# Performance work log

Hardware: AMD Instinct MI355X
Metric: run time of the kernel (lower is better)

## Reference

```python
import jax, jax.numpy as jnp
import numpy as np

K = 10
NUM_BLKS = 6
LN_EPS = 1e-6
NODE_D = 64


def layer_norm(x, g, b):
    m = jnp.mean(x, axis=-1, keepdims=True)
    v = jnp.var(x, axis=-1, keepdims=True)
    return (x - m) * jax.lax.rsqrt(v + LN_EPS) * g + b


def setup_inputs() -> dict:
    key = jax.random.key(0)
    B, N_c, N_t, D_S, D_F = 4, 4096, 1024, 3, 4
    D_IN = 4 + D_S + D_F  # obs-embed(4) + s + f
    ks = jax.random.split(key, 32)
    sc = 0.02
    inp = {
        "s_ctx": jax.random.normal(ks[0], (B, N_c, D_S), jnp.float32),
        "f_ctx": jax.random.normal(ks[1], (B, N_c, D_F), jnp.float32),
        "s_test": jax.random.normal(ks[2], (B, N_t, D_S), jnp.float32),
        "valid_lens_ctx": jax.random.randint(ks[3], (B,), N_c // 2, N_c + 1).astype(jnp.int32),
        # embed_obs: nn.Embed(2, 4)
        "emb_obs": jax.random.normal(ks[4], (2, 4), jnp.float32) * sc,
        # embed_all: MLP([256,128,64], gelu)
        "ea_W0": jax.random.normal(ks[5], (D_IN, 256), jnp.float32) * sc, "ea_b0": jnp.zeros((256,), jnp.float32),
        "ea_W1": jax.random.normal(ks[6], (256, 128), jnp.float32) * sc, "ea_b1": jnp.zeros((128,), jnp.float32),
        "ea_W2": jax.random.normal(ks[7], (128, NODE_D), jnp.float32) * sc, "ea_b2": jnp.zeros((NODE_D,), jnp.float32),
        # top-level LayerNorm
        "ln_g": jnp.ones((NODE_D,), jnp.float32), "ln_b": jnp.zeros((NODE_D,), jnp.float32),
        # GraphKRBlock params, stacked over NUM_BLKS blocks
        "blk_Wm0": jax.random.normal(ks[8], (NUM_BLKS, NODE_D + 1, 128), jnp.float32) * sc,
        "blk_bm0": jnp.zeros((NUM_BLKS, 128), jnp.float32),
        "blk_Wm1": jax.random.normal(ks[9], (NUM_BLKS, 128, NODE_D), jnp.float32) * sc,
        "blk_bm1": jnp.zeros((NUM_BLKS, NODE_D), jnp.float32),
        "blk_Wu0": jax.random.normal(ks[10], (NUM_BLKS, 2 * NODE_D, 128), jnp.float32) * sc,
        "blk_bu0": jnp.zeros((NUM_BLKS, 128), jnp.float32),
        "blk_Wu1": jax.random.normal(ks[11], (NUM_BLKS, 128, NODE_D), jnp.float32) * sc,
        "blk_bu1": jnp.zeros((NUM_BLKS, NODE_D), jnp.float32),
        "blk_lng": jnp.ones((NUM_BLKS, NODE_D), jnp.float32),
        "blk_lnb": jnp.zeros((NUM_BLKS, NODE_D), jnp.float32),
        # head: MLP([256,64,2], gelu)
        "hd_W0": jax.random.normal(ks[12], (NODE_D, 256), jnp.float32) * sc, "hd_b0": jnp.zeros((256,), jnp.float32),
        "hd_W1": jax.random.normal(ks[13], (256, 64), jnp.float32) * sc, "hd_b1": jnp.zeros((64,), jnp.float32),
        "hd_W2": jax.random.normal(ks[14], (64, 2), jnp.float32) * sc, "hd_b2": jnp.zeros((2,), jnp.float32),
    }
    return inp


def reference(s_ctx, f_ctx, s_test, valid_lens_ctx,
              emb_obs, ea_W0, ea_b0, ea_W1, ea_b1, ea_W2, ea_b2, ln_g, ln_b,
              blk_Wm0, blk_bm0, blk_Wm1, blk_bm1, blk_Wu0, blk_bu0, blk_Wu1, blk_bu1,
              blk_lng, blk_lnb, hd_W0, hd_b0, hd_W1, hd_b1, hd_W2, hd_b2):
    B, N_c, _ = s_ctx.shape
    N_t = s_test.shape[1]

    # --- per-sample O(n^2) KNN graph build (custom_k_nearest_senders, l2 dist) ---
    mask = jnp.arange(N_c)[None, :] < valid_lens_ctx[:, None]          # [B,N_c]
    s_send = jnp.where(mask[..., None], s_ctx, 1e6)                    # invalid -> far away
    rx = jnp.concatenate([s_ctx, s_test], axis=1)                      # [B,N,d_s] receivers
    d = jnp.sqrt(jnp.sum((rx[:, :, None, :] - s_send[:, None, :, :]) ** 2, axis=-1))  # [B,N,N_c]
    negd, senders = jax.lax.top_k(-d, K)                               # k-nearest: [B,N,K]
    dists = -negd                                                       # ascending distances

    # --- embeddings: stack(embed_obs, s, f) -> embed_all MLP -> LayerNorm ---
    def embed(x):
        h = jax.nn.gelu(x @ ea_W0 + ea_b0)
        h = jax.nn.gelu(h @ ea_W1 + ea_b1)
        h = h @ ea_W2 + ea_b2
        return layer_norm(h, ln_g, ln_b)

    ctx_in = jnp.concatenate(
        [jnp.broadcast_to(emb_obs[1], (B, N_c, emb_obs.shape[1])), s_ctx, f_ctx], axis=-1)
    test_in = jnp.concatenate(
        [jnp.broadcast_to(emb_obs[0], (B, N_t, emb_obs.shape[1])), s_test,
         jnp.zeros((B, N_t, f_ctx.shape[-1]), f_ctx.dtype)], axis=-1)
    nodes = jnp.concatenate([embed(ctx_in), embed(test_in)], axis=1)   # [B,N,64]

    # --- num_blks GraphKRBlock message-passing blocks ---
    bidx = jnp.arange(B)[:, None, None]
    w = jax.nn.softmax(-dists, axis=-1)                                # kernel weights per receiver
    for i in range(NUM_BLKS):
        sf = nodes[bidx, senders]                                      # gather senders [B,N,K,64]
        m_in = jnp.concatenate([sf, dists[..., None]], axis=-1)        # [B,N,K,65]
        m = jax.nn.gelu(m_in @ blk_Wm0[i] + blk_bm0[i]) @ blk_Wm1[i] + blk_bm1[i]
        agg = jnp.einsum('bnk,bnkd->bnd', w, m)                        # scatter-to-receivers
        u_in = jnp.concatenate([nodes, agg], axis=-1)                  # [B,N,128]
        upd = jax.nn.gelu(u_in @ blk_Wu0[i] + blk_bu0[i]) @ blk_Wu1[i] + blk_bu1[i]
        nodes = layer_norm(nodes + upd, blk_lng[i], blk_lnb[i])

    # --- head on test nodes ---
    x_t = nodes[:, N_c:, :]                                            # [B,N_t,64]
    h = jax.nn.gelu(x_t @ hd_W0 + hd_b0)
    h = jax.nn.gelu(h @ hd_W1 + hd_b1)
    f_dist = h @ hd_W2 + hd_b2                                         # [B,N_t,2]
    f_mu, f_log_var = jnp.split(f_dist, 2, axis=-1)
    f_std = jnp.exp(f_log_var / 2)                                     # min_std = 0.0
    return f_mu, f_std
```

## Files before the change

### kernel.cpp

```cpp
#include <hip/hip_runtime.h>
#include <math.h>

#define BB 4
#define NC 4096
#define NT 1024
#define NN (NC + NT)
#define NODES (BB * NN)
#define DD 64
#define KNN 10
#define NBLK 6
#define BIGF 3.0e38f

typedef __attribute__((ext_vector_type(8))) short short8;
typedef __attribute__((ext_vector_type(4))) float f32x4;
typedef __attribute__((ext_vector_type(4))) int int4v;

__device__ __forceinline__ unsigned short f2bf(float f) {
    unsigned int u = __float_as_uint(f);
    unsigned int r = (u + 0x7fffu + ((u >> 16) & 1u)) >> 16;
    return (unsigned short)r;
}
__device__ __forceinline__ float bf2f(unsigned short h) {
    return __uint_as_float(((unsigned int)h) << 16);
}

__device__ __forceinline__ float gelu_f(float x) {
    const float c0 = 0.7978845608028654f;
    float x3 = x * x * x;
    float z2 = 2.0f * c0 * (x + 0.044715f * x3);
    float e = __expf(z2);
    float r = __builtin_amdgcn_rcpf(1.0f + e);
    return x - x * r;
}

__device__ __forceinline__ float wave_sum(float v) {
#pragma unroll
    for (int off = 32; off > 0; off >>= 1) v += __shfl_xor(v, off, 64);
    return v;
}

__device__ __forceinline__ f32x4 mfma_bf16(short8 a, short8 b, f32x4 c) {
    asm("v_mfma_f32_16x16x32_bf16 %0, %1, %2, %0" : "+v"(c) : "v"(a), "v"(b));
    return c;
}


__global__ __launch_bounds__(256) void k_convw(
    const float* __restrict__ Wm0, const float* __restrict__ Wm1,
    const float* __restrict__ Wu0, const float* __restrict__ Wu1,
    const float* __restrict__ bm0,
    const float* __restrict__ eW0, const float* __restrict__ eW1,
    const float* __restrict__ eW2,
    const float* __restrict__ hW0, const float* __restrict__ hW1,
    const float* __restrict__ sctx,
    unsigned short* __restrict__ wtm0, unsigned short* __restrict__ wtm1p,
    unsigned short* __restrict__ wtu0, unsigned short* __restrict__ wtu1,
    float* __restrict__ wdp, float* __restrict__ bm0p,
    unsigned short* __restrict__ wte0, unsigned short* __restrict__ wte1,
    unsigned short* __restrict__ wte2,
    unsigned short* __restrict__ wth0, unsigned short* __restrict__ wth1,
    float4* __restrict__ s4)
{
    int t = blockIdx.x * 256 + threadIdx.x;
    if (t < 49152) {
        int i = t / 8192, r = t % 8192, n = r / 64, k = r % 64;
        wtm0[t] = f2bf(Wm0[(i * 65 + k) * 128 + n]);
    } else if (t < 98304) {
        int u = t - 49152;
        int i = u / 8192, r = u % 8192, n = r / 128, cp = r % 128;
        int col = ((cp & 7) << 4) | (cp >> 3);
        wtm1p[u] = f2bf(Wm1[(i * 128 + col) * 64 + n]);
    } else if (t < 196608) {
        int u = t - 98304;
        int i = u / 16384, r = u % 16384, n = r / 128, k = r % 128;
        wtu0[u] = f2bf(Wu0[(i * 128 + k) * 128 + n]);
    } else if (t < 245760) {
        int u = t - 196608;
        int i = u / 8192, r = u % 8192, n = r / 128, k = r % 128;
        wtu1[u] = f2bf(Wu1[(i * 128 + k) * 64 + n]);
    } else if (t < 246528) {
        int u = t - 245760;
        int i = u / 128, cp = u % 128;
        int col = ((cp & 7) << 4) | (cp >> 3);
        wdp[u] = Wm0[(i * 65 + 64) * 128 + col];
    } else if (t < 247296) {
        int u = t - 246528;
        int i = u / 128, cp = u % 128;
        int col = ((cp & 7) << 4) | (cp >> 3);
        bm0p[u] = bm0[i * 128 + col];
    } else if (t < 255488) {
        int u = t - 247296;
        int n = u / 32, k = u % 32;
        wte0[u] = (k < 11) ? f2bf(eW0[k * 256 + n]) : 0;
    } else if (t < 288256) {
        int u = t - 255488;
        int n = u / 256, k = u % 256;
        wte1[u] = f2bf(eW1[k * 128 + n]);
    } else if (t < 296448) {
        int u = t - 288256;
        int n = u / 128, k = u % 128;
        wte2[u] = f2bf(eW2[k * 64 + n]);
    } else if (t < 312832) {
        int u = t - 296448;
        int n = u / 64, k = u % 64;
        wth0[u] = f2bf(hW0[k * 256 + n]);
    } else if (t < 329216) {
        int u = t - 312832;
        int n = u / 256, k = u % 256;
        wth1[u] = f2bf(hW1[k * 64 + n]);
    } else if (t < 329216 + BB * NC) {
        int u = t - 329216;
        float x = sctx[u * 3], y = sctx[u * 3 + 1], z = sctx[u * 3 + 2];
        s4[u] = make_float4(x, y, z, 0.0f);
    }
}

__global__ __launch_bounds__(256) void k_embed2(
    const float* __restrict__ s_ctx, const float* __restrict__ f_ctx,
    const float* __restrict__ s_test, const float* __restrict__ emb_obs,
    const unsigned short* __restrict__ WT0, const float* __restrict__ b0,
    const unsigned short* __restrict__ WT1, const float* __restrict__ b1,
    const unsigned short* __restrict__ WT2, const float* __restrict__ b2,
    const float* __restrict__ g, const float* __restrict__ bta,
    const unsigned short* __restrict__ Wm0n,
    unsigned short* __restrict__ nodes,
    unsigned short* __restrict__ Pout)
{
    __shared__ unsigned short H0[4][16 * 256];
    __shared__ unsigned short H1[4][16 * 128];
    __shared__ unsigned short XO[4][16 * 64];
    int t = threadIdx.x;
    int wave = t >> 6, lane = t & 63, lr = lane & 15, lk = lane >> 4;
    int rb = wave * 16;
    int n0 = blockIdx.x * 64;
    int bq = n0 / NN, nloc0 = n0 % NN;
    bool is_ctx = nloc0 < NC;
    int nr = nloc0 + rb + lr;
    float xv[8];
#pragma unroll
    for (int j = 0; j < 8; ++j) xv[j] = 0.0f;
    if (lk == 0) {
        const float* eb = emb_obs + (is_ctx ? 4 : 0);
        xv[0] = eb[0]; xv[1] = eb[1]; xv[2] = eb[2]; xv[3] = eb[3];
        if (is_ctx) {
            const float* sp = s_ctx + ((size_t)(bq * NC + nr)) * 3;
            const float* fp = f_ctx + ((size_t)(bq * NC + nr)) * 4;
            xv[4] = sp[0]; xv[5] = sp[1]; xv[6] = sp[2]; xv[7] = fp[0];
        } else {
            const float* sp = s_test + ((size_t)(bq * NT + nr - NC)) * 3;
            xv[4] = sp[0]; xv[5] = sp[1]; xv[6] = sp[2];
        }
    } else if (lk == 1 && is_ctx) {
        const float* fp = f_ctx + ((size_t)(bq * NC + nr)) * 4;
        xv[0] = fp[1]; xv[1] = fp[2]; xv[2] = fp[3];
    }
    short8 a;
#pragma unroll
    for (int j = 0; j < 8; ++j) a[j] = (short)f2bf(xv[j]);

    f32x4 acc0[16];
#pragma unroll
    for (int nt = 0; nt < 16; ++nt) {
        short8 bb = *(const short8*)(WT0 + (nt * 16 + lr) * 32 + lk * 8);
        f32x4 z = (f32x4){0.f, 0.f, 0.f, 0.f};
        acc0[nt] = mfma_bf16(a, bb, z);
    }
    unsigned short* h0 = &H0[wave][0];
#pragma unroll
    for (int nt = 0; nt < 16; ++nt) {
        int col = nt * 16 + lr;
        float bias = b0[col];
        int u = col >> 3;
#pragma unroll
        for (int j = 0; j < 4; ++j) {
            int row = lk * 4 + j;
            float v = gelu_f(acc0[nt][j] + bias);
            int us = (u & 16) | ((u ^ row) & 15);
            h0[row * 256 + us * 8 + (col & 7)] = f2bf(v);
        }
    }
    f32x4 acc1[8];
#pragma unroll
    for (int nt = 0; nt < 8; ++nt) acc1[nt] = (f32x4){0.f, 0.f, 0.f, 0.f};
#pragma unroll
    for (int ks = 0; ks < 8; ++ks) {
        int u = ks * 4 + lk;
        int us = (u & 16) | ((u ^ lr) & 15);
        short8 aa = *(const short8*)(&h0[lr * 256 + us * 8]);
#pragma unroll
        for (int nt = 0; nt < 8; ++nt) {
            short8 bb = *(const short8*)(WT1 + (nt * 16 + lr) * 256 + ks * 32 + lk * 8);
            acc1[nt] = mfma_bf16(aa, bb, acc1[nt]);
        }
    }
    unsigned short* h1 = &H1[wave][0];
#pragma unroll
    for (int nt = 0; nt < 8; ++nt) {
        int col = nt * 16 + lr;
        float bias = b1[col];
        int u = col >> 3;
#pragma unroll
        for (int j = 0; j < 4; ++j) {
            int row = lk * 4 + j;
            float v = gelu_f(acc1[nt][j] + bias);
            int us = (u ^ row) & 15;
            h1[row * 128 + us * 8 + (col & 7)] = f2bf(v);
        }
    }
    f32x4 acc2[4];
#pragma unroll
    for (int nt = 0; nt < 4; ++nt) acc2[nt] = (f32x4){0.f, 0.f, 0.f, 0.f};
#pragma unroll
    for (int ks = 0; ks < 4; ++ks) {
        int u = ks * 4 + lk;
        int us = (u ^ lr) & 15;
        short8 aa = *(const short8*)(&h1[lr * 128 + us * 8]);
#pragma unroll
        for (int nt = 0; nt < 4; ++nt) {
            short8 bb = *(const short8*)(WT2 + (nt * 16 + lr) * 128 + ks * 32 + lk * 8);
            acc2[nt] = mfma_bf16(aa, bb, acc2[nt]);
        }
    }
    float vals[4][4];
#pragma unroll
    for (int j = 0; j < 4; ++j)
#pragma unroll
        for (int nt = 0; nt < 4; ++nt)
            vals[j][nt] = acc2[nt][j] + b2[nt * 16 + lr];
    unsigned short* xo = &XO[wave][0];
#pragma unroll
    for (int j = 0; j < 4; ++j) {
        float s = vals[j][0] + vals[j][1] + vals[j][2] + vals[j][3];
#pragma unroll
        for (int m = 1; m < 16; m <<= 1) s += __shfl_xor(s, m, 64);
        float mean = s * (1.0f / 64.0f);
        float vs = 0.0f;
#pragma unroll
        for (int nt = 0; nt < 4; ++nt) { float d = vals[j][nt] - mean; vs += d * d; }
#pragma unroll
        for (int m = 1; m < 16; m <<= 1) vs += __shfl_xor(vs, m, 64);
        float inv = rsqrtf(vs * (1.0f / 64.0f) + 1e-6f);
        int row = lk * 4 + j;
        int node = n0 + rb + row;
#pragma unroll
        for (int nt = 0; nt < 4; ++nt) {
            int col = nt * 16 + lr;
            float o = (vals[j][nt] - mean) * inv * g[col] + bta[col];
            unsigned short ob = f2bf(o);
            nodes[(size_t)node * 64 + col] = ob;
            xo[row * 64 + ((col >> 3) ^ (row & 7)) * 8 + (col & 7)] = ob;
        }
    }
    f32x4 accP[8];
#pragma unroll
    for (int nt = 0; nt < 8; ++nt) accP[nt] = (f32x4){0.f, 0.f, 0.f, 0.f};
#pragma unroll
    for (int ks = 0; ks < 2; ++ks) {
        short8 aa = *(const short8*)(&xo[lr * 64 + ((ks * 4 + lk) ^ (lr & 7)) * 8]);
#pragma unroll
        for (int nt = 0; nt < 8; ++nt) {
            short8 bb = *(const short8*)(Wm0n + (nt * 16 + lr) * 64 + ks * 32 + lk * 8);
            accP[nt] = mfma_bf16(aa, bb, accP[nt]);
        }
    }
#pragma unroll
    for (int j = 0; j < 4; ++j) {
        int node = n0 + rb + lk * 4 + j;
        short8 ps;
#pragma unroll
        for (int nt = 0; nt < 8; ++nt) ps[nt] = (short)f2bf(accP[nt][j]);
        *(short8*)(Pout + (size_t)node * 128 + lr * 8) = ps;
    }
}

__global__ __launch_bounds__(256) void k_topk(
    const float4* __restrict__ s4, const float* __restrict__ s_ctx,
    const float* __restrict__ s_test, const int* __restrict__ valid_lens,
    float* __restrict__ dists, int* __restrict__ senders, float* __restrict__ wout)
{
    __shared__ float cd[4 * 64 * 11];
    __shared__ float seld[4][4][12];
    __shared__ int   seli[4][4][12];
    __shared__ int   eqis[4][4][12];
    int wave = threadIdx.x >> 6;
    int lane = threadIdx.x & 63;
    int r0 = blockIdx.x * 16 + wave * 4;
    int b = r0 / NN;
    int vl = valid_lens[b];
    const float4* sc = s4 + (size_t)b * NC;
    float px[4], py[4], pz[4];
#pragma unroll
    for (int q = 0; q < 4; ++q) {
        int n = (r0 + q) % NN;
        const float* p = (n < NC) ? &s_ctx[(size_t)(b * NC + n) * 3]
                                  : &s_test[(size_t)(b * NT + (n - NC)) * 3];
        px[q] = p[0]; py[q] = p[1]; pz[q] = p[2];
    }
    float bq[4][KNN];
#pragma unroll
    for (int q = 0; q < 4; ++q)
#pragma unroll
        for (int k = 0; k < KNN; ++k) bq[q][k] = BIGF;
#pragma unroll 8
    for (int i = 0; i < 64; ++i) {
        int j = lane + (i << 6);
        float4 s = sc[j];
        bool ok = j < vl;
#pragma unroll
        for (int q = 0; q < 4; ++q) {
            float dx = px[q] - s.x, dy = py[q] - s.y, dz = pz[q] - s.z;
            float d2 = fmaf(dx, dx, fmaf(dy, dy, dz * dz));
            d2 = ok ? d2 : BIGF;
#pragma unroll
            for (int k = KNN - 1; k >= 1; --k)
                bq[q][k] = __builtin_amdgcn_fmed3f(bq[q][k - 1], bq[q][k], d2);
            bq[q][0] = fminf(bq[q][0], d2);
        }
    }
    int base = (wave * 64 + lane) * 11;
    float T[4], dmin[4];
    int m[4];
#pragma unroll
    for (int q = 0; q < 4; ++q) {
#pragma unroll
        for (int k = 0; k < KNN; ++k) cd[base + k] = bq[q][k];
        __builtin_amdgcn_wave_barrier();
        int head = 0;
        float myd = 0.0f;
#pragma unroll
        for (int rr = 0; rr < KNN; ++rr) {
            float v = cd[base + head];
            float mv = v;
#pragma unroll
            for (int off = 32; off > 0; off >>= 1) mv = fminf(mv, __shfl_xor(mv, off, 64));
            unsigned long long ball = __ballot(v == mv);
            int win = __ffsll(ball) - 1;
            if (lane == win) head++;
            if (lane == rr) myd = mv;
        }
        T[q] = __shfl(myd, 9, 64);
        dmin[q] = sqrtf(__shfl(myd, 0, 64));
        m[q] = __popcll(__ballot(lane < KNN && myd < T[q]));
    }
    unsigned long long below = (lane == 63) ? 0x7FFFFFFFFFFFFFFFull
                                            : ((1ull << lane) - 1);
    int cless[4] = {0, 0, 0, 0}, ceq[4] = {0, 0, 0, 0};
#pragma unroll 4
    for (int i = 0; i < 64; ++i) {
        int j = lane + (i << 6);
        float4 s = sc[j];
        bool ok = j < vl;
#pragma unroll
        for (int q = 0; q < 4; ++q) {
            float dx = px[q] - s.x, dy = py[q] - s.y, dz = pz[q] - s.z;
            float v = fmaf(dx, dx, fmaf(dy, dy, dz * dz));
            v = ok ? v : BIGF;
            unsigned long long ml = __ballot(v < T[q]);
            unsigned long long me = __ballot(v == T[q]);
            if (v < T[q]) {
                int slot = cless[q] + __popcll(ml & below);
                if (slot < 12) { seld[wave][q][slot] = v; seli[wave][q][slot] = j; }
            }
            if (v == T[q]) {
                int qq = ceq[q] + __popcll(me & below);
                if (qq < 12) eqis[wave][q][qq] = j;
            }
            cless[q] += __popcll(ml);
            ceq[q] += __popcll(me);
        }
    }
    __builtin_amdgcn_wave_barrier();
#pragma unroll
    for (int q = 0; q < 4; ++q) {
        float e = 0.0f, d = 0.0f;
        int isel = 0;
        if (lane < KNN) {
            float vsel;
            if (lane < m[q]) { vsel = seld[wave][q][lane]; isel = seli[wave][q][lane]; }
            else             { vsel = T[q];                isel = eqis[wave][q][lane - m[q]]; }
            d = sqrtf(vsel);
            e = __expf(-(d - dmin[q]));
        }
        float ssum = wave_sum(e);
        if (lane < KNN) {
            size_t o = (size_t)(r0 + q) * KNN + lane;
            dists[o] = d;
            senders[o] = isel;
            wout[o] = e / ssum;
        }
    }
}

__global__ __launch_bounds__(256) void k_blk(
    const unsigned short* __restrict__ nodes_in,
    const unsigned short* __restrict__ P,
    const float* __restrict__ dists, const int* __restrict__ senders,
    const float* __restrict__ w,
    const float* __restrict__ wdp, const float* __restrict__ bm0p,
    const unsigned short* __restrict__ Wm1p,
    const float* __restrict__ bm1,
    const unsigned short* __restrict__ WTu0,
    const float* __restrict__ bu0,
    const unsigned short* __restrict__ WTu1,
    const float* __restrict__ bu1,
    const float* __restrict__ lng, const float* __restrict__ lnb,
    const unsigned short* __restrict__ Wm0n,
    const int doP,
    unsigned short* __restrict__ nodes_out,
    unsigned short* __restrict__ Pout)
{
    __shared__ unsigned short X[16 * 64];
    __shared__ unsigned short G[16 * 128];
    __shared__ unsigned short AG[16 * 64];
    __shared__ unsigned short H[16 * 128];
    __shared__ unsigned short XO[16 * 64];
    __shared__ int   sidE[160];
    __shared__ float dE[160], wE[160];
    int l = threadIdx.x;
    int wave = l >> 6, lane = l & 63;
    int n0 = blockIdx.x * 16;
    int b = n0 / NN;
    size_t bbase = (size_t)b * NN;
    int e0 = n0 * KNN;
    if (l < 160) {
        sidE[l] = senders[e0 + l];
        dE[l]   = dists[e0 + l];
        wE[l]   = w[e0 + l];
    }
    if (l < 128) {
        int row = l >> 3, u = l & 7;
        int4v v = *(const int4v*)(nodes_in + ((size_t)(n0 + row)) * 64 + u * 8);
        *(int4v*)(&X[row * 64 + (u ^ (row & 7)) * 8]) = v;
    }
    __syncthreads();
    float wd0 = wdp[2 * lane], wd1 = wdp[2 * lane + 1];
    float bb0 = bm0p[2 * lane], bb1 = bm0p[2 * lane + 1];
    const unsigned int* Pb = (const unsigned int*)P;
    unsigned int* G32 = (unsigned int*)G;
#pragma unroll
    for (int nn = 0; nn < 4; ++nn) {
        int n = wave * 4 + nn;
        float a0 = 0.0f, a1 = 0.0f;
#pragma unroll
        for (int k = 0; k < KNN; ++k) {
            int e = n * KNN + k;
            int sid = sidE[e];
            float dd = dE[e], ww = wE[e];
            unsigned int pr = Pb[(bbase + sid) * 64 + lane];
// ... 95 lines not shown
        for (int mm = 1; mm < 16; mm <<= 1) vs += __shfl_xor(vs, mm, 64);
        float inv = rsqrtf(vs * (1.0f / 64.0f) + 1e-6f);
#pragma unroll
        for (int nt = 0; nt < 4; ++nt) {
            int col = nt * 16 + lr;
            float o = (vals[j][nt] - mean) * inv * lng[col] + lnb[col];
            unsigned short ob = f2bf(o);
            nodes_out[((size_t)(n0 + row)) * 64 + col] = ob;
            XO[row * 64 + ((col >> 3) ^ (row & 7)) * 8 + (col & 7)] = ob;
        }
    }
    if (doP) {
        f32x4 accP[8];
#pragma unroll
        for (int nt = 0; nt < 8; ++nt) accP[nt] = (f32x4){0.f, 0.f, 0.f, 0.f};
#pragma unroll
        for (int ks = 0; ks < 2; ++ks) {
            short8 aa = *(const short8*)(&XO[lr * 64 + ((ks * 4 + lk) ^ (lr & 7)) * 8]);
#pragma unroll
            for (int nt = 0; nt < 8; ++nt) {
                short8 bb = *(const short8*)(Wm0n + (nt * 16 + lr) * 64 + ks * 32 + lk * 8);
                accP[nt] = mfma_bf16(aa, bb, accP[nt]);
            }
        }
#pragma unroll
        for (int j = 0; j < 4; ++j) {
            int node = n0 + lk * 4 + j;
            short8 ps;
#pragma unroll
            for (int nt = 0; nt < 8; ++nt) ps[nt] = (short)f2bf(accP[nt][j]);
            *(short8*)(Pout + (size_t)node * 128 + lr * 8) = ps;
        }
    }
}

__global__ __launch_bounds__(256) void k_head2(
    const unsigned short* __restrict__ nodes,
    const unsigned short* __restrict__ WT0, const float* __restrict__ b0,
    const unsigned short* __restrict__ WT1, const float* __restrict__ b1,
    const float* __restrict__ W2, const float* __restrict__ b2,
    float* __restrict__ out)
{
    __shared__ unsigned short H0[4][16 * 256];
    __shared__ unsigned short H1[4][16 * 72];
    int t = threadIdx.x;
    int wave = t >> 6, lane = t & 63, lr = lane & 15, lk = lane >> 4;
    int rb = wave * 16;
    int n0 = blockIdx.x * 64;
    int bq = n0 / NT, nloc0 = n0 % NT;
    size_t grow = (size_t)(bq * NN + NC + nloc0 + rb);
    short8 a0 = *(const short8*)(nodes + (grow + lr) * 64 + lk * 8);
    short8 a1 = *(const short8*)(nodes + (grow + lr) * 64 + 32 + lk * 8);
    f32x4 acc0[16];
#pragma unroll
    for (int nt = 0; nt < 16; ++nt) {
        short8 bb0 = *(const short8*)(WT0 + (nt * 16 + lr) * 64 + lk * 8);
        short8 bb1 = *(const short8*)(WT0 + (nt * 16 + lr) * 64 + 32 + lk * 8);
        f32x4 z = (f32x4){0.f, 0.f, 0.f, 0.f};
        z = mfma_bf16(a0, bb0, z);
        acc0[nt] = mfma_bf16(a1, bb1, z);
    }
    unsigned short* h0 = &H0[wave][0];
#pragma unroll
    for (int nt = 0; nt < 16; ++nt) {
        int col = nt * 16 + lr;
        float bias = b0[col];
        int u = col >> 3;
#pragma unroll
        for (int j = 0; j < 4; ++j) {
            int row = lk * 4 + j;
            float v = gelu_f(acc0[nt][j] + bias);
            int us = (u & 16) | ((u ^ row) & 15);
            h0[row * 256 + us * 8 + (col & 7)] = f2bf(v);
        }
    }
    f32x4 acc1[4];
#pragma unroll
    for (int nt = 0; nt < 4; ++nt) acc1[nt] = (f32x4){0.f, 0.f, 0.f, 0.f};
#pragma unroll
    for (int ks = 0; ks < 8; ++ks) {
        int u = ks * 4 + lk;
        int us = (u & 16) | ((u ^ lr) & 15);
        short8 aa = *(const short8*)(&h0[lr * 256 + us * 8]);
#pragma unroll
        for (int nt = 0; nt < 4; ++nt) {
            short8 bb = *(const short8*)(WT1 + (nt * 16 + lr) * 256 + ks * 32 + lk * 8);
            acc1[nt] = mfma_bf16(aa, bb, acc1[nt]);
        }
    }
    unsigned short* h1 = &H1[wave][0];
#pragma unroll
    for (int nt = 0; nt < 4; ++nt) {
        int col = nt * 16 + lr;
        float bias = b1[col];
#pragma unroll
        for (int j = 0; j < 4; ++j) {
            int row = lk * 4 + j;
            h1[row * 72 + col] = f2bf(gelu_f(acc1[nt][j] + bias));
        }
    }
    int task = lane >> 1;
    int row = task >> 1;
    int o = task & 1;
    int t2 = lane & 1;
    float p = 0.0f;
#pragma unroll
    for (int d = 0; d < 32; ++d) {
        int dd = t2 * 32 + d;
        p += bf2f(h1[row * 72 + dd]) * W2[dd * 2 + o];
    }
    p += __shfl_xor(p, 1, 64);
    if (t2 == 0) {
        int gg = n0 + rb + row;
        if (o == 0) out[gg] = p + b2[0];
        else        out[BB * NT + gg] = __expf(0.5f * (p + b2[1]));
    }
}

extern "C" void kernel_launch(void* const* d_in, const int* in_sizes, int n_in,
                              void* d_out, int out_size, void* d_ws, size_t ws_size,
                              hipStream_t stream)
{
    (void)in_sizes; (void)n_in; (void)out_size; (void)ws_size;
    const float* s_ctx   = (const float*)d_in[0];
    const float* f_ctx   = (const float*)d_in[1];
    const float* s_test  = (const float*)d_in[2];
    const int*   valid   = (const int*)d_in[3];
    const float* emb_obs = (const float*)d_in[4];
    const float* ea_W0   = (const float*)d_in[5];
    const float* ea_b0   = (const float*)d_in[6];
    const float* ea_W1   = (const float*)d_in[7];
    const float* ea_b1   = (const float*)d_in[8];
    const float* ea_W2   = (const float*)d_in[9];
    const float* ea_b2   = (const float*)d_in[10];
    const float* ln_g    = (const float*)d_in[11];
    const float* ln_b    = (const float*)d_in[12];
    const float* blk_Wm0 = (const float*)d_in[13];
    const float* blk_bm0 = (const float*)d_in[14];
    const float* blk_Wm1 = (const float*)d_in[15];
    const float* blk_bm1 = (const float*)d_in[16];
    const float* blk_Wu0 = (const float*)d_in[17];
    const float* blk_bu0 = (const float*)d_in[18];
    const float* blk_Wu1 = (const float*)d_in[19];
    const float* blk_bu1 = (const float*)d_in[20];
    const float* blk_lng = (const float*)d_in[21];
    const float* blk_lnb = (const float*)d_in[22];
    const float* hd_W0   = (const float*)d_in[23];
    const float* hd_b0   = (const float*)d_in[24];
    const float* hd_W1   = (const float*)d_in[25];
    const float* hd_b1   = (const float*)d_in[26];
    const float* hd_W2   = (const float*)d_in[27];
    const float* hd_b2   = (const float*)d_in[28];

    char* p = (char*)d_ws;
    auto alloc = [&](size_t bytes) { char* r = p; p += (bytes + 255) & ~(size_t)255; return r; };
    unsigned short* nodesA = (unsigned short*)alloc((size_t)NODES * 64 * 2);
    unsigned short* nodesB = (unsigned short*)alloc((size_t)NODES * 64 * 2);
    unsigned short* Pbuf   = (unsigned short*)alloc((size_t)NODES * 128 * 2);
    float* dists   = (float*)alloc((size_t)NODES * KNN * 4);
    float* wbuf    = (float*)alloc((size_t)NODES * KNN * 4);
    int*   senders = (int*)alloc((size_t)NODES * KNN * 4);
    unsigned short* wtm0  = (unsigned short*)alloc((size_t)6 * 8192 * 2);
    unsigned short* wtm1p = (unsigned short*)alloc((size_t)6 * 8192 * 2);
    unsigned short* wtu0  = (unsigned short*)alloc((size_t)6 * 16384 * 2);
    unsigned short* wtu1  = (unsigned short*)alloc((size_t)6 * 8192 * 2);
    float* wdp  = (float*)alloc((size_t)6 * 128 * 4);
    float* bm0p = (float*)alloc((size_t)6 * 128 * 4);
    unsigned short* wte0 = (unsigned short*)alloc((size_t)8192 * 2);
    unsigned short* wte1 = (unsigned short*)alloc((size_t)32768 * 2);
    unsigned short* wte2 = (unsigned short*)alloc((size_t)8192 * 2);
    unsigned short* wth0 = (unsigned short*)alloc((size_t)16384 * 2);
    unsigned short* wth1 = (unsigned short*)alloc((size_t)16384 * 2);
    float4* s4 = (float4*)alloc((size_t)BB * NC * 16);

    k_convw<<<1350, 256, 0, stream>>>(
        blk_Wm0, blk_Wm1, blk_Wu0, blk_Wu1, blk_bm0,
        ea_W0, ea_W1, ea_W2, hd_W0, hd_W1, s_ctx,
        wtm0, wtm1p, wtu0, wtu1, wdp, bm0p, wte0, wte1, wte2, wth0, wth1, s4);

    k_embed2<<<NODES / 64, 256, 0, stream>>>(s_ctx, f_ctx, s_test, emb_obs,
        wte0, ea_b0, wte1, ea_b1, wte2, ea_b2, ln_g, ln_b, wtm0, nodesA, Pbuf);

    k_topk<<<NODES / 16, 256, 0, stream>>>(s4, s_ctx, s_test, valid,
                                           dists, senders, wbuf);

    unsigned short* nin = nodesA; unsigned short* nout = nodesB;
    for (int i = 0; i < NBLK; ++i) {
        int doP = (i < NBLK - 1) ? 1 : 0;
        const unsigned short* wm0n = wtm0 + (size_t)((i + 1) % NBLK) * 8192;
        k_blk<<<NODES / 16, 256, 0, stream>>>(nin, Pbuf, dists, senders, wbuf,
            wdp + (size_t)i * 128, bm0p + (size_t)i * 128,
            wtm1p + (size_t)i * 8192, blk_bm1 + (size_t)i * 64,
            wtu0 + (size_t)i * 16384, blk_bu0 + (size_t)i * 128,
            wtu1 + (size_t)i * 8192, blk_bu1 + (size_t)i * 64,
            blk_lng + (size_t)i * 64, blk_lnb + (size_t)i * 64,
            wm0n, doP, nout, Pbuf);
        unsigned short* tmp = nin; nin = nout; nout = tmp;
    }

    k_head2<<<BB * NT / 64, 256, 0, stream>>>(nin, wth0, hd_b0, wth1, hd_b1,
                                              hd_W2, hd_b2, (float*)d_out);
}
```

Baseline: 304.9 us.

## Fuse embed and top-k into one front kernel; fold head into last block

```diff
diff --git a/kernel.cpp b/kernel.cpp
--- a/kernel.cpp
+++ b/kernel.cpp
@@ -52,7 +52,7 @@
     const float* __restrict__ eW0, const float* __restrict__ eW1,
     const float* __restrict__ eW2,
     const float* __restrict__ hW0, const float* __restrict__ hW1,
-    const float* __restrict__ sctx,
+    const float* __restrict__ sctx, const int* __restrict__ valid_lens,
     unsigned short* __restrict__ wtm0, unsigned short* __restrict__ wtm1p,
     unsigned short* __restrict__ wtu0, unsigned short* __restrict__ wtu1,
     float* __restrict__ wdp, float* __restrict__ bm0p,
@@ -110,12 +110,17 @@
         wth1[u] = f2bf(hW1[k * 64 + n]);
     } else if (t < 329216 + BB * NC) {
         int u = t - 329216;
-        float x = sctx[u * 3], y = sctx[u * 3 + 1], z = sctx[u * 3 + 2];
+        int b = u / NC, j = u % NC;
+        bool ok = j < valid_lens[b];
+        float x = ok ? sctx[u * 3] : 1.0e6f;
+        float y = ok ? sctx[u * 3 + 1] : 1.0e6f;
+        float z = ok ? sctx[u * 3 + 2] : 1.0e6f;
         s4[u] = make_float4(x, y, z, 0.0f);
     }
 }
 
-__global__ __launch_bounds__(256) void k_embed2(
+__global__ __launch_bounds__(256) void k_front(
+    const float4* __restrict__ s4,
     const float* __restrict__ s_ctx, const float* __restrict__ f_ctx,
     const float* __restrict__ s_test, const float* __restrict__ emb_obs,
     const unsigned short* __restrict__ WT0, const float* __restrict__ b0,
@@ -124,269 +129,271 @@
     const float* __restrict__ g, const float* __restrict__ bta,
     const unsigned short* __restrict__ Wm0n,
     unsigned short* __restrict__ nodes,
-    unsigned short* __restrict__ Pout)
+    unsigned short* __restrict__ Pout,
+    float* __restrict__ dists, int* __restrict__ senders,
+    float* __restrict__ wout)
 {
-    __shared__ unsigned short H0[4][16 * 256];
-    __shared__ unsigned short H1[4][16 * 128];
-    __shared__ unsigned short XO[4][16 * 64];
+    __shared__ int4v SMv[2048];
+    char* SM = (char*)SMv;
+    int rblk = blockIdx.x;
     int t = threadIdx.x;
-    int wave = t >> 6, lane = t & 63, lr = lane & 15, lk = lane >> 4;
-    int rb = wave * 16;
-    int n0 = blockIdx.x * 64;
-    int bq = n0 / NN, nloc0 = n0 % NN;
-    bool is_ctx = nloc0 < NC;
-    int nr = nloc0 + rb + lr;
-    float xv[8];
-#pragma unroll
-    for (int j = 0; j < 8; ++j) xv[j] = 0.0f;
-    if (lk == 0) {
-        const float* eb = emb_obs + (is_ctx ? 4 : 0);
-        xv[0] = eb[0]; xv[1] = eb[1]; xv[2] = eb[2]; xv[3] = eb[3];
-        if (is_ctx) {
-            const float* sp = s_ctx + ((size_t)(bq * NC + nr)) * 3;
+    int wave = t >> 6, lane = t & 63;
+
+    if ((rblk % 5) != 4) {
+        int bid = rblk - (rblk + 1) / 5;
+        float* cd = (float*)SM;
+        float (*seld)[4][12] = (float (*)[4][12])(SM + 11264);
+        int   (*seli)[4][12] = (int (*)[4][12])(SM + 12032);
+        int   (*eqis)[4][12] = (int (*)[4][12])(SM + 12800);
+        int r0 = bid * 16 + wave * 4;
+        int b = r0 / NN;
+        const float4* sc = s4 + (size_t)b * NC;
+        float px[4], py[4], pz[4];
+#pragma unroll
+        for (int q = 0; q < 4; ++q) {
+            int n = (r0 + q) % NN;
+            const float* p = (n < NC) ? &s_ctx[(size_t)(b * NC + n) * 3]
+                                      : &s_test[(size_t)(b * NT + (n - NC)) * 3];
+            px[q] = p[0]; py[q] = p[1]; pz[q] = p[2];
+        }
+        float bq[4][KNN];
+#pragma unroll
+        for (int q = 0; q < 4; ++q)
+#pragma unroll
+            for (int k = 0; k < KNN; ++k) bq[q][k] = BIGF;
+#pragma unroll 8
+        for (int i = 0; i < 64; ++i) {
+            int j = lane + (i << 6);
+            float4 s = sc[j];
+#pragma unroll
+            for (int q = 0; q < 4; ++q) {
+                float dx = px[q] - s.x, dy = py[q] - s.y, dz = pz[q] - s.z;
+                float d2 = fmaf(dx, dx, fmaf(dy, dy, dz * dz));
+#pragma unroll
+                for (int k = KNN - 1; k >= 1; --k)
+                    bq[q][k] = __builtin_amdgcn_fmed3f(bq[q][k - 1], bq[q][k], d2);
+                bq[q][0] = fminf(bq[q][0], d2);
+            }
+        }
+        int base = (wave * 64 + lane) * 11;
+        float T[4], dmin[4];
+        int m[4];
+#pragma unroll
+        for (int q = 0; q < 4; ++q) {
+#pragma unroll
+            for (int k = 0; k < KNN; ++k) cd[base + k] = bq[q][k];
+            __builtin_amdgcn_wave_barrier();
+            int head = 0;
+            float myd = 0.0f;
+#pragma unroll
+            for (int rr = 0; rr < KNN; ++rr) {
+                float v = cd[base + head];
+                float mv = v;
+#pragma unroll
+                for (int off = 32; off > 0; off >>= 1) mv = fminf(mv, __shfl_xor(mv, off, 64));
+                unsigned long long ball = __ballot(v == mv);
+                int win = __ffsll(ball) - 1;
+                if (lane == win) head++;
+                if (lane == rr) myd = mv;
+            }
+            T[q] = __shfl(myd, 9, 64);
+            dmin[q] = sqrtf(__shfl(myd, 0, 64));
+            m[q] = __popcll(__ballot(lane < KNN && myd < T[q]));
+        }
+        unsigned long long below = (lane == 63) ? 0x7FFFFFFFFFFFFFFFull
+                                                : ((1ull << lane) - 1);
+        int cless[4] = {0, 0, 0, 0}, ceq[4] = {0, 0, 0, 0};
+#pragma unroll 4
+        for (int i = 0; i < 64; ++i) {
+            int j = lane + (i << 6);
+            float4 s = sc[j];
+#pragma unroll
+            for (int q = 0; q < 4; ++q) {
+                float dx = px[q] - s.x, dy = py[q] - s.y, dz = pz[q] - s.z;
+                float v = fmaf(dx, dx, fmaf(dy, dy, dz * dz));
+                unsigned long long ml = __ballot(v < T[q]);
+                unsigned long long me = __ballot(v == T[q]);
+                if (v < T[q]) {
+                    int slot = cless[q] + __popcll(ml & below);
+                    if (slot < 12) { seld[wave][q][slot] = v; seli[wave][q][slot] = j; }
+                }
+                if (v == T[q]) {
+                    int qq = ceq[q] + __popcll(me & below);
+                    if (qq < 12) eqis[wave][q][qq] = j;
+                }
+                cless[q] += __popcll(ml);
+                ceq[q] += __popcll(me);
+            }
+        }
+        __builtin_amdgcn_wave_barrier();
+#pragma unroll
+        for (int q = 0; q < 4; ++q) {
+            float e = 0.0f, d = 0.0f;
+            int isel = 0;
+            if (lane < KNN) {
+                float vsel;
+                if (lane < m[q]) { vsel = seld[wave][q][lane]; isel = seli[wave][q][lane]; }
+                else             { vsel = T[q];                isel = eqis[wave][q][lane - m[q]]; }
+                d = sqrtf(vsel);
+                e = __expf(-(d - dmin[q]));
+            }
+            float ssum = wave_sum(e);
+            if (lane < KNN) {
+                size_t o = (size_t)(r0 + q) * KNN + lane;
+                dists[o] = d;
+                senders[o] = isel;
+                wout[o] = e / ssum;
+            }
+        }
+        return;
+    }
+
+    {
+        int bid = rblk / 5;
+        int lr = lane & 15, lk = lane >> 4;
+        int rb = wave * 16;
+        int n0 = bid * 64;
+        int bq = n0 / NN, nloc0 = n0 % NN;
+        bool is_ctx = nloc0 < NC;
+        int nr = nloc0 + rb + lr;
+        unsigned short* h0 = (unsigned short*)SM + wave * 4096;
+        unsigned short* h1 = h0;
+        unsigned short* xo = h0;
+        float xv[8];
+#pragma unroll
+        for (int j = 0; j < 8; ++j) xv[j] = 0.0f;
+        if (lk == 0) {
+            const float* eb = emb_obs + (is_ctx ? 4 : 0);
+            xv[0] = eb[0]; xv[1] = eb[1]; xv[2] = eb[2]; xv[3] = eb[3];
+            if (is_ctx) {
+                const float* sp = s_ctx + ((size_t)(bq * NC + nr)) * 3;
+                const float* fp = f_ctx + ((size_t)(bq * NC + nr)) * 4;
+                xv[4] = sp[0]; xv[5] = sp[1]; xv[6] = sp[2]; xv[7] = fp[0];
+            } else {
+                const float* sp = s_test + ((size_t)(bq * NT + nr - NC)) * 3;
+                xv[4] = sp[0]; xv[5] = sp[1]; xv[6] = sp[2];
+            }
+        } else if (lk == 1 && is_ctx) {
             const float* fp = f_ctx + ((size_t)(bq * NC + nr)) * 4;
-            xv[4] = sp[0]; xv[5] = sp[1]; xv[6] = sp[2]; xv[7] = fp[0];
-        } else {
-            const float* sp = s_test + ((size_t)(bq * NT + nr - NC)) * 3;
-            xv[4] = sp[0]; xv[5] = sp[1]; xv[6] = sp[2];
-        }
-    } else if (lk == 1 && is_ctx) {
-        const float* fp = f_ctx + ((size_t)(bq * NC + nr)) * 4;
-        xv[0] = fp[1]; xv[1] = fp[2]; xv[2] = fp[3];
-    }
-    short8 a;
-#pragma unroll
-    for (int j = 0; j < 8; ++j) a[j] = (short)f2bf(xv[j]);
-
-    f32x4 acc0[16];
-#pragma unroll
-    for (int nt = 0; nt < 16; ++nt) {
-        short8 bb = *(const short8*)(WT0 + (nt * 16 + lr) * 32 + lk * 8);
-        f32x4 z = (f32x4){0.f, 0.f, 0.f, 0.f};
-        acc0[nt] = mfma_bf16(a, bb, z);
-    }
-    unsigned short* h0 = &H0[wave][0];
-#pragma unroll
-    for (int nt = 0; nt < 16; ++nt) {
-        int col = nt * 16 + lr;
-        float bias = b0[col];
-        int u = col >> 3;
+            xv[0] = fp[1]; xv[1] = fp[2]; xv[2] = fp[3];
+        }
+        short8 a;
+#pragma unroll
+        for (int j = 0; j < 8; ++j) a[j] = (short)f2bf(xv[j]);
+
+#pragma unroll
+        for (int half = 0; half < 2; ++half) {
+            f32x4 acc0[8];
+#pragma unroll
+            for (int nt = 0; nt < 8; ++nt) {
+                int col16 = half * 8 + nt;
+                short8 bb = *(const short8*)(WT0 + (col16 * 16 + lr) * 32 + lk * 8);
+                f32x4 z = (f32x4){0.f, 0.f, 0.f, 0.f};
+                acc0[nt] = mfma_bf16(a, bb, z);
+            }
+#pragma unroll
+            for (int nt = 0; nt < 8; ++nt) {
+                int col = (half * 8 + nt) * 16 + lr;
+                float bias = b0[col];
+                int u = col >> 3;
+#pragma unroll
+                for (int j = 0; j < 4; ++j) {
+                    int row = lk * 4 + j;
+                    float v = gelu_f(acc0[nt][j] + bias);
+                    int us = (u & 16) | ((u ^ row) & 15);
+                    h0[row * 256 + us * 8 + (col & 7)] = f2bf(v);
+                }
+            }
+        }
+        f32x4 acc1[8];
+#pragma unroll
+        for (int nt = 0; nt < 8; ++nt) acc1[nt] = (f32x4){0.f, 0.f, 0.f, 0.f};
+#pragma unroll
+        for (int ks = 0; ks < 8; ++ks) {
+            int u = ks * 4 + lk;
+            int us = (u & 16) | ((u ^ lr) & 15);
+            short8 aa = *(const short8*)(&h0[lr * 256 + us * 8]);
+#pragma unroll
+            for (int nt = 0; nt < 8; ++nt) {
+                short8 bb = *(const short8*)(WT1 + (nt * 16 + lr) * 256 + ks * 32 + lk * 8);
+                acc1[nt] = mfma_bf16(aa, bb, acc1[nt]);
+            }
+        }
+#pragma unroll
+        for (int nt = 0; nt < 8; ++nt) {
+            int col = nt * 16 + lr;
+            float bias = b1[col];
+            int u = col >> 3;
+#pragma unroll
+            for (int j = 0; j < 4; ++j) {
+                int row = lk * 4 + j;
+                float v = gelu_f(acc1[nt][j] + bias);
+                int us = (u ^ row) & 15;
+                h1[row * 128 + us * 8 + (col & 7)] = f2bf(v);
+            }
+        }
+        f32x4 acc2[4];
+#pragma unroll
+        for (int nt = 0; nt < 4; ++nt) acc2[nt] = (f32x4){0.f, 0.f, 0.f, 0.f};
+#pragma unroll
+        for (int ks = 0; ks < 4; ++ks) {
+            int u = ks * 4 + lk;
+            int us = (u ^ lr) & 15;
+            short8 aa = *(const short8*)(&h1[lr * 128 + us * 8]);
+#pragma unroll
+            for (int nt = 0; nt < 4; ++nt) {
+                short8 bb = *(const short8*)(WT2 + (nt * 16 + lr) * 128 + ks * 32 + lk * 8);
+                acc2[nt] = mfma_bf16(aa, bb, acc2[nt]);
+            }
+        }
+        float vals[4][4];
+#pragma unroll
+        for (int j = 0; j < 4; ++j)
+#pragma unroll
+            for (int nt = 0; nt < 4; ++nt)
+                vals[j][nt] = acc2[nt][j] + b2[nt * 16 + lr];
 #pragma unroll
         for (int j = 0; j < 4; ++j) {
+            float s = vals[j][0] + vals[j][1] + vals[j][2] + vals[j][3];
+#pragma unroll
+            for (int mm = 1; mm < 16; mm <<= 1) s += __shfl_xor(s, mm, 64);
+            float mean = s * (1.0f / 64.0f);
+            float vs = 0.0f;
+#pragma unroll
+            for (int nt = 0; nt < 4; ++nt) { float d = vals[j][nt] - mean; vs += d * d; }
+#pragma unroll
+            for (int mm = 1; mm < 16; mm <<= 1) vs += __shfl_xor(vs, mm, 64);
+            float inv = rsqrtf(vs * (1.0f / 64.0f) + 1e-6f);
             int row = lk * 4 + j;
-            float v = gelu_f(acc0[nt][j] + bias);
-            int us = (u & 16) | ((u ^ row) & 15);
-            h0[row * 256 + us * 8 + (col & 7)] = f2bf(v);
-        }
-    }
-    f32x4 acc1[8];
-#pragma unroll
-    for (int nt = 0; nt < 8; ++nt) acc1[nt] = (f32x4){0.f, 0.f, 0.f, 0.f};
-#pragma unroll
-    for (int ks = 0; ks < 8; ++ks) {
-        int u = ks * 4 + lk;
-        int us = (u & 16) | ((u ^ lr) & 15);
-        short8 aa = *(const short8*)(&h0[lr * 256 + us * 8]);
-#pragma unroll
-        for (int nt = 0; nt < 8; ++nt) {
-            short8 bb = *(const short8*)(WT1 + (nt * 16 + lr) * 256 + ks * 32 + lk * 8);
-            acc1[nt] = mfma_bf16(aa, bb, acc1[nt]);
-        }
-    }
-    unsigned short* h1 = &H1[wave][0];
-#pragma unroll
-    for (int nt = 0; nt < 8; ++nt) {
-        int col = nt * 16 + lr;
-        float bias = b1[col];
-        int u = col >> 3;
+            int node = n0 + rb + row;
+#pragma unroll
+            for (int nt = 0; nt < 4; ++nt) {
+                int col = nt * 16 + lr;
+                float o = (vals[j][nt] - mean) * inv * g[col] + bta[col];
+                unsigned short ob = f2bf(o);
+                nodes[(size_t)node * 64 + col] = ob;
+                xo[row * 64 + ((col >> 3) ^ (row & 7)) * 8 + (col & 7)] = ob;
+            }
+        }
+        f32x4 accP[8];
+#pragma unroll
+        for (int nt = 0; nt < 8; ++nt) accP[nt] = (f32x4){0.f, 0.f, 0.f, 0.f};
+#pragma unroll
+        for (int ks = 0; ks < 2; ++ks) {
+            short8 aa = *(const short8*)(&xo[lr * 64 + ((ks * 4 + lk) ^ (lr & 7)) * 8]);
+#pragma unroll
+            for (int nt = 0; nt < 8; ++nt) {
+                short8 bb = *(const short8*)(Wm0n + (nt * 16 + lr) * 64 + ks * 32 + lk * 8);
+                accP[nt] = mfma_bf16(aa, bb, accP[nt]);
+            }
+        }
 #pragma unroll
         for (int j = 0; j < 4; ++j) {
-            int row = lk * 4 + j;
-            float v = gelu_f(acc1[nt][j] + bias);
-            int us = (u ^ row) & 15;
-            h1[row * 128 + us * 8 + (col & 7)] = f2bf(v);
-        }
-    }
-    f32x4 acc2[4];
-#pragma unroll
-    for (int nt = 0; nt < 4; ++nt) acc2[nt] = (f32x4){0.f, 0.f, 0.f, 0.f};
-#pragma unroll
-    for (int ks = 0; ks < 4; ++ks) {
-        int u = ks * 4 + lk;
-        int us = (u ^ lr) & 15;
-        short8 aa = *(const short8*)(&h1[lr * 128 + us * 8]);
-#pragma unroll
-        for (int nt = 0; nt < 4; ++nt) {
-            short8 bb = *(const short8*)(WT2 + (nt * 16 + lr) * 128 + ks * 32 + lk * 8);
-            acc2[nt] = mfma_bf16(aa, bb, acc2[nt]);
-        }
-    }
-    float vals[4][4];
-#pragma unroll
-    for (int j = 0; j < 4; ++j)
-#pragma unroll
-        for (int nt = 0; nt < 4; ++nt)
-            vals[j][nt] = acc2[nt][j] + b2[nt * 16 + lr];
-    unsigned short* xo = &XO[wave][0];
-#pragma unroll
-    for (int j = 0; j < 4; ++j) {
-        float s = vals[j][0] + vals[j][1] + vals[j][2] + vals[j][3];
-#pragma unroll
-        for (int m = 1; m < 16; m <<= 1) s += __shfl_xor(s, m, 64);
-        float mean = s * (1.0f / 64.0f);
-        float vs = 0.0f;
-#pragma unroll
-        for (int nt = 0; nt < 4; ++nt) { float d = vals[j][nt] - mean; vs += d * d; }
-#pragma unroll
-        for (int m = 1; m < 16; m <<= 1) vs += __shfl_xor(vs, m, 64);
-        float inv = rsqrtf(vs * (1.0f / 64.0f) + 1e-6f);
-        int row = lk * 4 + j;
-        int node = n0 + rb + row;
-#pragma unroll
-        for (int nt = 0; nt < 4; ++nt) {
-            int col = nt * 16 + lr;
-            float o = (vals[j][nt] - mean) * inv * g[col] + bta[col];
-            unsigned short ob = f2bf(o);
-            nodes[(size_t)node * 64 + col] = ob;
-            xo[row * 64 + ((col >> 3) ^ (row & 7)) * 8 + (col & 7)] = ob;
-        }
-    }
-    f32x4 accP[8];
-#pragma unroll
-    for (int nt = 0; nt < 8; ++nt) accP[nt] = (f32x4){0.f, 0.f, 0.f, 0.f};
-#pragma unroll
-    for (int ks = 0; ks < 2; ++ks) {
-        short8 aa = *(const short8*)(&xo[lr * 64 + ((ks * 4 + lk) ^ (lr & 7)) * 8]);
-#pragma unroll
-        for (int nt = 0; nt < 8; ++nt) {
-            short8 bb = *(const short8*)(Wm0n + (nt * 16 + lr) * 64 + ks * 32 + lk * 8);
-            accP[nt] = mfma_bf16(aa, bb, accP[nt]);
-        }
-    }
-#pragma unroll
-    for (int j = 0; j < 4; ++j) {
-        int node = n0 + rb + lk * 4 + j;
-        short8 ps;
-#pragma unroll
-        for (int nt = 0; nt < 8; ++nt) ps[nt] = (short)f2bf(accP[nt][j]);
-        *(short8*)(Pout + (size_t)node * 128 + lr * 8) = ps;
-    }
-}
-
-__global__ __launch_bounds__(256) void k_topk(
-    const float4* __restrict__ s4, const float* __restrict__ s_ctx,
-    const float* __restrict__ s_test, const int* __restrict__ valid_lens,
-    float* __restrict__ dists, int* __restrict__ senders, float* __restrict__ wout)
-{
-    __shared__ float cd[4 * 64 * 11];
-    __shared__ float seld[4][4][12];
-    __shared__ int   seli[4][4][12];
-    __shared__ int   eqis[4][4][12];
-    int wave = threadIdx.x >> 6;
-    int lane = threadIdx.x & 63;
-    int r0 = blockIdx.x * 16 + wave * 4;
-    int b = r0 / NN;
-    int vl = valid_lens[b];
-    const float4* sc = s4 + (size_t)b * NC;
-    float px[4], py[4], pz[4];
-#pragma unroll
-    for (int q = 0; q < 4; ++q) {
-        int n = (r0 + q) % NN;
-        const float* p = (n < NC) ? &s_ctx[(size_t)(b * NC + n) * 3]
-                                  : &s_test[(size_t)(b * NT + (n - NC)) * 3];
-        px[q] = p[0]; py[q] = p[1]; pz[q] = p[2];
-    }
-    float bq[4][KNN];
-#pragma unroll
-    for (int q = 0; q < 4; ++q)
-#pragma unroll
-        for (int k = 0; k < KNN; ++k) bq[q][k] = BIGF;
-#pragma unroll 8
-    for (int i = 0; i < 64; ++i) {
-        int j = lane + (i << 6);
-        float4 s = sc[j];
-        bool ok = j < vl;
-#pragma unroll
-        for (int q = 0; q < 4; ++q) {
-            float dx = px[q] - s.x, dy = py[q] - s.y, dz = pz[q] - s.z;
-            float d2 = fmaf(dx, dx, fmaf(dy, dy, dz * dz));
-            d2 = ok ? d2 : BIGF;
-#pragma unroll
-            for (int k = KNN - 1; k >= 1; --k)
-                bq[q][k] = __builtin_amdgcn_fmed3f(bq[q][k - 1], bq[q][k], d2);
-            bq[q][0] = fminf(bq[q][0], d2);
-        }
-    }
-    int base = (wave * 64 + lane) * 11;
-    float T[4], dmin[4];
-    int m[4];
-#pragma unroll
-    for (int q = 0; q < 4; ++q) {
-#pragma unroll
-        for (int k = 0; k < KNN; ++k) cd[base + k] = bq[q][k];
-        __builtin_amdgcn_wave_barrier();
-        int head = 0;
-        float myd = 0.0f;
-#pragma unroll
-        for (int rr = 0; rr < KNN; ++rr) {
-            float v = cd[base + head];
-            float mv = v;
-#pragma unroll
-            for (int off = 32; off > 0; off >>= 1) mv = fminf(mv, __shfl_xor(mv, off, 64));
-            unsigned long long ball = __ballot(v == mv);
-            int win = __ffsll(ball) - 1;
-            if (lane == win) head++;
-            if (lane == rr) myd = mv;
-        }
-        T[q] = __shfl(myd, 9, 64);
-        dmin[q] = sqrtf(__shfl(myd, 0, 64));
-        m[q] = __popcll(__ballot(lane < KNN && myd < T[q]));
-    }
-    unsigned long long below = (lane == 63) ? 0x7FFFFFFFFFFFFFFFull
-                                            : ((1ull << lane) - 1);
-    int cless[4] = {0, 0, 0, 0}, ceq[4] = {0, 0, 0, 0};
-#pragma unroll 4
-    for (int i = 0; i < 64; ++i) {
-        int j = lane + (i << 6);
-        float4 s = sc[j];
-        bool ok = j < vl;
-#pragma unroll
-        for (int q = 0; q < 4; ++q) {
-            float dx = px[q] - s.x, dy = py[q] - s.y, dz = pz[q] - s.z;
-            float v = fmaf(dx, dx, fmaf(dy, dy, dz * dz));
-            v = ok ? v : BIGF;
-            unsigned long long ml = __ballot(v < T[q]);
-            unsigned long long me = __ballot(v == T[q]);
-            if (v < T[q]) {
-                int slot = cless[q] + __popcll(ml & below);
-                if (slot < 12) { seld[wave][q][slot] = v; seli[wave][q][slot] = j; }
-            }
-            if (v == T[q]) {
-                int qq = ceq[q] + __popcll(me & below);
-                if (qq < 12) eqis[wave][q][qq] = j;
-            }
-            cless[q] += __popcll(ml);
-            ceq[q] += __popcll(me);
-        }
-    }
-    __builtin_amdgcn_wave_barrier();
-#pragma unroll
-    for (int q = 0; q < 4; ++q) {
-        float e = 0.0f, d = 0.0f;
-        int isel = 0;
-        if (lane < KNN) {
-            float vsel;
-            if (lane < m[q]) { vsel = seld[wave][q][lane]; isel = seli[wave][q][lane]; }
-            else             { vsel = T[q];                isel = eqis[wave][q][lane - m[q]]; }
-            d = sqrtf(vsel);
-            e = __expf(-(d - dmin[q]));
-        }
-        float ssum = wave_sum(e);
-        if (lane < KNN) {
-            size_t o = (size_t)(r0 + q) * KNN + lane;
-            dists[o] = d;
-            senders[o] = isel;
-            wout[o] = e / ssum;
+            int node = n0 + rb + lk * 4 + j;
+            short8 ps;
+#pragma unroll
+            for (int nt = 0; nt < 8; ++nt) ps[nt] = (short)f2bf(accP[nt][j]);
+            *(short8*)(Pout + (size_t)node * 128 + lr * 8) = ps;
         }
     }
 }
@@ -407,13 +414,22 @@
     const unsigned short* __restrict__ Wm0n,
     const int doP,
     unsigned short* __restrict__ nodes_out,
-    unsigned short* __restrict__ Pout)
+    unsigned short* __restrict__ Pout,
+    const int doHead,
+    const unsigned short* __restrict__ wth0,
+    const float* __restrict__ hb0,
+    const unsigned short* __restrict__ wth1,
+    const float* __restrict__ hb1,
+    const float* __restrict__ hW2, const float* __restrict__ hb2,
+    float* __restrict__ out)
 {
     __shared__ unsigned short X[16 * 64];
     __shared__ unsigned short G[16 * 128];
     __shared__ unsigned short AG[16 * 64];
     __shared__ unsigned short H[16 * 128];
     __shared__ unsigned short XO[16 * 64];
+    __shared__ unsigned short HH[16 * 256];
+    __shared__ unsigned short HH1[16 * 72];
     __shared__ int   sidE[160];
     __shared__ float dE[160], wE[160];
     int l = threadIdx.x;
@@ -575,88 +591,78 @@
             *(short8*)(Pout + (size_t)node * 128 + lr * 8) = ps;
         }
     }
-}
-
-__global__ __launch_bounds__(256) void k_head2(
-    const unsigned short* __restrict__ nodes,
-    const unsigned short* __restrict__ WT0, const float* __restrict__ b0,
-    const unsigned short* __restrict__ WT1, const float* __restrict__ b1,
-    const float* __restrict__ W2, const float* __restrict__ b2,
-    float* __restrict__ out)
-{
-    __shared__ unsigned short H0[4][16 * 256];
-    __shared__ unsigned short H1[4][16 * 72];
-    int t = threadIdx.x;
-    int wave = t >> 6, lane = t & 63, lr = lane & 15, lk = lane >> 4;
-    int rb = wave * 16;
-    int n0 = blockIdx.x * 64;
-    int bq = n0 / NT, nloc0 = n0 % NT;
-    size_t grow = (size_t)(bq * NN + NC + nloc0 + rb);
-    short8 a0 = *(const short8*)(nodes + (grow + lr) * 64 + lk * 8);
-    short8 a1 = *(const short8*)(nodes + (grow + lr) * 64 + 32 + lk * 8);
-    f32x4 acc0[16];
-#pragma unroll
-    for (int nt = 0; nt < 16; ++nt) {
-        short8 bb0 = *(const short8*)(WT0 + (nt * 16 + lr) * 64 + lk * 8);
-        short8 bb1 = *(const short8*)(WT0 + (nt * 16 + lr) * 64 + 32 + lk * 8);
-        f32x4 z = (f32x4){0.f, 0.f, 0.f, 0.f};
-        z = mfma_bf16(a0, bb0, z);
-        acc0[nt] = mfma_bf16(a1, bb1, z);
-    }
-    unsigned short* h0 = &H0[wave][0];
-#pragma unroll
-    for (int nt = 0; nt < 16; ++nt) {
-        int col = nt * 16 + lr;
-        float bias = b0[col];
-        int u = col >> 3;
-#pragma unroll
-        for (int j = 0; j < 4; ++j) {
-            int row = lk * 4 + j;
-            float v = gelu_f(acc0[nt][j] + bias);
-            int us = (u & 16) | ((u ^ row) & 15);
-            h0[row * 256 + us * 8 + (col & 7)] = f2bf(v);
-        }
-    }
-    f32x4 acc1[4];
-#pragma unroll
-    for (int nt = 0; nt < 4; ++nt) acc1[nt] = (f32x4){0.f, 0.f, 0.f, 0.f};
-#pragma unroll
-    for (int ks = 0; ks < 8; ++ks) {
-        int u = ks * 4 + lk;
-        int us = (u & 16) | ((u ^ lr) & 15);
-        short8 aa = *(const short8*)(&h0[lr * 256 + us * 8]);
+    int nloc = n0 % NN;
+    if (doHead && nloc >= NC) {
+        int bq = n0 / NN;
+#pragma unroll
+        for (int half = 0; half < 2; ++half) {
+            f32x4 ah[8];
+#pragma unroll
+            for (int nt = 0; nt < 8; ++nt) ah[nt] = (f32x4){0.f, 0.f, 0.f, 0.f};
+#pragma unroll
+            for (int ks = 0; ks < 2; ++ks) {
+                short8 aa = *(const short8*)(&XO[lr * 64 + ((ks * 4 + lk) ^ (lr & 7)) * 8]);
+#pragma unroll
+                for (int nt = 0; nt < 8; ++nt) {
+                    int col16 = half * 8 + nt;
+                    short8 bb = *(const short8*)(wth0 + (col16 * 16 + lr) * 64 + ks * 32 + lk * 8);
+                    ah[nt] = mfma_bf16(aa, bb, ah[nt]);
+                }
+            }
+#pragma unroll
+            for (int nt = 0; nt < 8; ++nt) {
+                int col = (half * 8 + nt) * 16 + lr;
+                float bias = hb0[col];
+                int u = col >> 3;
+#pragma unroll
+                for (int j = 0; j < 4; ++j) {
+                    int row = lk * 4 + j;
+                    float v = gelu_f(ah[nt][j] + bias);
+                    int us = (u & 16) | ((u ^ row) & 15);
+                    HH[row * 256 + us * 8 + (col & 7)] = f2bf(v);
+                }
+            }
+        }
+        f32x4 a1h[4];
+#pragma unroll
+        for (int nt = 0; nt < 4; ++nt) a1h[nt] = (f32x4){0.f, 0.f, 0.f, 0.f};
+#pragma unroll
+        for (int ks = 0; ks < 8; ++ks) {
+            int u = ks * 4 + lk;
+            int us = (u & 16) | ((u ^ lr) & 15);
+            short8 aa = *(const short8*)(&HH[lr * 256 + us * 8]);
+#pragma unroll
+            for (int nt = 0; nt < 4; ++nt) {
+                short8 bb = *(const short8*)(wth1 + (nt * 16 + lr) * 256 + ks * 32 + lk * 8);
+                a1h[nt] = mfma_bf16(aa, bb, a1h[nt]);
+            }
+        }
 #pragma unroll
         for (int nt = 0; nt < 4; ++nt) {
-            short8 bb = *(const short8*)(WT1 + (nt * 16 + lr) * 256 + ks * 32 + lk * 8);
-            acc1[nt] = mfma_bf16(aa, bb, acc1[nt]);
-        }
-    }
-    unsigned short* h1 = &H1[wave][0];
-#pragma unroll
-    for (int nt = 0; nt < 4; ++nt) {
-        int col = nt * 16 + lr;
-        float bias = b1[col];
-#pragma unroll
-        for (int j = 0; j < 4; ++j) {
-            int row = lk * 4 + j;
-            h1[row * 72 + col] = f2bf(gelu_f(acc1[nt][j] + bias));
-        }
-    }
-    int task = lane >> 1;
-    int row = task >> 1;
-    int o = task & 1;
-    int t2 = lane & 1;
-    float p = 0.0f;
-#pragma unroll
-    for (int d = 0; d < 32; ++d) {
-        int dd = t2 * 32 + d;
-        p += bf2f(h1[row * 72 + dd]) * W2[dd * 2 + o];
-    }
-    p += __shfl_xor(p, 1, 64);
-    if (t2 == 0) {
-        int gg = n0 + rb + row;
-        if (o == 0) out[gg] = p + b2[0];
-        else        out[BB * NT + gg] = __expf(0.5f * (p + b2[1]));
+            int col = nt * 16 + lr;
+            float bias = hb1[col];
+#pragma unroll
+            for (int j = 0; j < 4; ++j) {
+                int row = lk * 4 + j;
+                HH1[row * 72 + col] = f2bf(gelu_f(a1h[nt][j] + bias));
+            }
+        }
+        int task = lane >> 1;
+        int row = task >> 1;
+        int o = task & 1;
+        int t2 = lane & 1;
+        float pp = 0.0f;
+#pragma unroll
+        for (int d = 0; d < 32; ++d) {
+            int dd = t2 * 32 + d;
+            pp += bf2f(HH1[row * 72 + dd]) * hW2[dd * 2 + o];
+        }
+        pp += __shfl_xor(pp, 1, 64);
+        if (t2 == 0) {
+            int gg = bq * NT + (nloc - NC) + row;
+            if (o == 0) out[gg] = pp + hb2[0];
+            else        out[BB * NT + gg] = __expf(0.5f * (pp + hb2[1]));
+        }
     }
 }
 
@@ -718,18 +724,17 @@
 
     k_convw<<<1350, 256, 0, stream>>>(
         blk_Wm0, blk_Wm1, blk_Wu0, blk_Wu1, blk_bm0,
-        ea_W0, ea_W1, ea_W2, hd_W0, hd_W1, s_ctx,
+        ea_W0, ea_W1, ea_W2, hd_W0, hd_W1, s_ctx, valid,
         wtm0, wtm1p, wtu0, wtu1, wdp, bm0p, wte0, wte1, wte2, wth0, wth1, s4);
 
-    k_embed2<<<NODES / 64, 256, 0, stream>>>(s_ctx, f_ctx, s_test, emb_obs,
-        wte0, ea_b0, wte1, ea_b1, wte2, ea_b2, ln_g, ln_b, wtm0, nodesA, Pbuf);
-
-    k_topk<<<NODES / 16, 256, 0, stream>>>(s4, s_ctx, s_test, valid,
-                                           dists, senders, wbuf);
+    k_front<<<1600, 256, 0, stream>>>(s4, s_ctx, f_ctx, s_test, emb_obs,
+        wte0, ea_b0, wte1, ea_b1, wte2, ea_b2, ln_g, ln_b, wtm0,
+        nodesA, Pbuf, dists, senders, wbuf);
 
     unsigned short* nin = nodesA; unsigned short* nout = nodesB;
     for (int i = 0; i < NBLK; ++i) {
         int doP = (i < NBLK - 1) ? 1 : 0;
+        int doHead = (i == NBLK - 1) ? 1 : 0;
         const unsigned short* wm0n = wtm0 + (size_t)((i + 1) % NBLK) * 8192;
         k_blk<<<NODES / 16, 256, 0, stream>>>(nin, Pbuf, dists, senders, wbuf,
             wdp + (size_t)i * 128, bm0p + (size_t)i * 128,
@@ -737,10 +742,8 @@
             wtu0 + (size_t)i * 16384, blk_bu0 + (size_t)i * 128,
             wtu1 + (size_t)i * 8192, blk_bu1 + (size_t)i * 64,
             blk_lng + (size_t)i * 64, blk_lnb + (size_t)i * 64,
-            wm0n, doP, nout, Pbuf);
+            wm0n, doP, nout, Pbuf,
+            doHead, wth0, hd_b0, wth1, hd_b1, hd_W2, hd_b2, (float*)d_out);
         unsigned short* tmp = nin; nin = nout; nout = tmp;
     }
-
-    k_head2<<<BB * NT / 64, 256, 0, stream>>>(nin, wth0, hd_b0, wth1, hd_b1,
-                                              hd_W2, hd_b2, (float*)d_out);
-}
+}
```

Result: slower. 331.6 us (+8.8%).
